# Kernel optimization log

Hardware: AMD Instinct MI355X
Metric: run time of the kernel (lower is better)

The kernel has to match this reference:

```python
import jax, jax.numpy as jnp
import numpy as np

B, L, N, D = 128, 256, 64, 1024  # batch, text_len, img_num, feat size (text=obj=place=D)


def masked_softmax(logits, mask=None):
    # matches MaskedSoftmax(dim=1): softmax over last axis, then renormalize by mask
    dist = jax.nn.softmax(logits, axis=-1)
    if mask is None:
        return dist
    dist = dist * mask
    return dist / jnp.sum(dist, axis=-1, keepdims=True)


def setup_inputs() -> dict:
    key = jax.random.key(0)
    ks = jax.random.split(key, 32)
    s = lambda d: 1.0 / np.sqrt(d)
    inp = {
        'text_feat': jax.random.normal(ks[0], (B, D), jnp.float32),
        'text_feats': jax.random.normal(ks[1], (B, L, D), jnp.float32),
        'img_object_feat': jax.random.normal(ks[2], (B, D), jnp.float32),
        'img_object_feats': jax.random.normal(ks[3], (B, N, D), jnp.float32),
        'img_place_feat': jax.random.normal(ks[4], (B, D), jnp.float32),
        'img_place_feats': jax.random.normal(ks[5], (B, N, D), jnp.float32),
        'src_mask': (jax.random.uniform(ks[6], (B, L)) < 0.9).astype(jnp.float32).at[:, 0].set(1.0),
        # score vectors (nn.Linear(D,1,bias=False))
        'v_to': jax.random.uniform(ks[7], (D,), jnp.float32, -s(D), s(D)),
        'v_tp': jax.random.uniform(ks[8], (D,), jnp.float32, -s(D), s(D)),
        'v_io': jax.random.uniform(ks[9], (D,), jnp.float32, -s(D), s(D)),
        'v_ip': jax.random.uniform(ks[10], (D,), jnp.float32, -s(D), s(D)),
        # cross-modal projections (bias=False), torch layout [out,in]
        'W_t2o': jax.random.uniform(ks[11], (D, D), jnp.float32, -s(D), s(D)),
        'W_t2p': jax.random.uniform(ks[12], (D, D), jnp.float32, -s(D), s(D)),
        'W_o2t': jax.random.uniform(ks[13], (D, D), jnp.float32, -s(D), s(D)),
        'W_p2t': jax.random.uniform(ks[14], (D, D), jnp.float32, -s(D), s(D)),
        # self projections with bias
        'W_oo': jax.random.uniform(ks[15], (D, D), jnp.float32, -s(D), s(D)),
        'b_oo': jax.random.uniform(ks[16], (D,), jnp.float32, -s(D), s(D)),
        'W_pp': jax.random.uniform(ks[17], (D, D), jnp.float32, -s(D), s(D)),
        'b_pp': jax.random.uniform(ks[18], (D,), jnp.float32, -s(D), s(D)),
        'W_tot': jax.random.uniform(ks[19], (D, D), jnp.float32, -s(D), s(D)),
        'b_tot': jax.random.uniform(ks[20], (D,), jnp.float32, -s(D), s(D)),
        'W_tpt': jax.random.uniform(ks[21], (D, D), jnp.float32, -s(D), s(D)),
        'b_tpt': jax.random.uniform(ks[22], (D,), jnp.float32, -s(D), s(D)),
        # output linear: in = 2*D + D + D = 4D
        'W_out': jax.random.uniform(ks[23], (D, 4 * D), jnp.float32, -s(4 * D), s(4 * D)),
        'b_out': jax.random.uniform(ks[24], (D,), jnp.float32, -s(4 * D), s(4 * D)),
    }
    return inp


def _text_att_ctx(text_feat, img_feats, W_img2text, W_text, b_text, v):
    # additive attention of text over image regions
    e = jnp.tanh(jnp.einsum('bnd,td->bnt', img_feats, W_img2text)
                 + (text_feat @ W_text.T + b_text)[:, None, :])
    scores = jnp.einsum('bnt,t->bn', e, v)
    dist = masked_softmax(scores)
    return jnp.einsum('bn,bnd->bd', dist, img_feats)


def _img_att_ctx(img_feat, text_feats, W_text2img, W_img, b_img, v, mask):
    e = jnp.tanh(jnp.einsum('bld,id->bli', text_feats, W_text2img)
                 + (img_feat @ W_img.T + b_img)[:, None, :])
    scores = jnp.einsum('bli,i->bl', e, v)
    dist = masked_softmax(scores, mask)
    return jnp.einsum('bl,bld->bd', dist, text_feats)


def reference(text_feat, text_feats, img_object_feat, img_object_feats, img_place_feat,
              img_place_feats, src_mask, v_to, v_tp, v_io, v_ip, W_t2o, W_t2p, W_o2t,
              W_p2t, W_oo, b_oo, W_pp, b_pp, W_tot, b_tot, W_tpt, b_tpt, W_out, b_out):
    img_object_context = _text_att_ctx(text_feat, img_object_feats, W_o2t, W_tot, b_tot, v_to)
    img_place_context = _text_att_ctx(text_feat, img_place_feats, W_p2t, W_tpt, b_tpt, v_tp)
    text_object_context = _img_att_ctx(img_object_feat, text_feats, W_t2o, W_oo, b_oo, v_io, src_mask)
    text_place_context = _img_att_ctx(img_place_feat, text_feats, W_t2p, W_pp, b_pp, v_ip, src_mask)
    combined = jnp.concatenate([img_object_context, img_place_context,
                                text_object_context, text_place_context], axis=1)
    # dropout is identity at inference
    return combined @ W_out.T + b_out
```

## Files before the change

### kernel.cpp

```cpp
#include <hip/hip_runtime.h>
#include <hip/hip_bf16.h>

typedef __attribute__((ext_vector_type(8))) short bf16x8;
typedef __attribute__((ext_vector_type(4))) float f32x4;

__device__ __forceinline__ uint pack_bf16x2(float a, float b) {
    __hip_bfloat162 p = __float22bfloat162_rn(make_float2(a, b));
    union { __hip_bfloat162 h; uint u; } c; c.h = p; return c.u;
}
__device__ __forceinline__ float bfu(ushort u) { return __uint_as_float(((uint)u) << 16); }

__device__ __forceinline__ float fast_tanh(float x) {
    float e = __expf(2.f * x);
    return 1.f - 2.f * __builtin_amdgcn_rcpf(e + 1.f);
}

__device__ __forceinline__ float wredmax(float v) {
    #pragma unroll
    for (int o = 32; o; o >>= 1) v = fmaxf(v, __shfl_xor(v, o, 64));
    return v;
}
__device__ __forceinline__ float wredsum(float v) {
    #pragma unroll
    for (int o = 32; o; o >>= 1) v += __shfl_xor(v, o, 64);
    return v;
}

__device__ __forceinline__ void gload16(const void* g, void* l) {
    __builtin_amdgcn_global_load_lds(
        (const __attribute__((address_space(1))) void*)g,
        (__attribute__((address_space(3))) void*)l, 16, 0, 0);
}

struct CvtTab {
    const float* src[8];
    ushort* dst[8];
    unsigned cum[9];
};

__global__ void cvt_bf16(CvtTab t, unsigned total4) {
    unsigned stride = gridDim.x * blockDim.x;
    for (unsigned i = blockIdx.x * blockDim.x + threadIdx.x; i < total4; i += stride) {
        int j = 0;
        while (i >= t.cum[j + 1]) ++j;
        unsigned off = i - t.cum[j];
        float4 v = reinterpret_cast<const float4*>(t.src[j])[off];
        uint2 o;
        o.x = pack_bf16x2(v.x, v.y);
        o.y = pack_bf16x2(v.z, v.w);
        reinterpret_cast<uint2*>(t.dst[j])[off] = o;
    }
}

struct Cvt8Tab {
    const float* src[8];
    uchar* dst[8];
    unsigned cum[9];
};

__device__ __forceinline__ uint pk8(float4 v) {
    int r = __builtin_amdgcn_cvt_pk_fp8_f32(v.x, v.y, 0, false);
    r = __builtin_amdgcn_cvt_pk_fp8_f32(v.z, v.w, r, true);
    return (uint)r;
}

__global__ void cvt_fp8(Cvt8Tab t, unsigned total16) {
    unsigned stride = gridDim.x * blockDim.x;
    for (unsigned i = blockIdx.x * blockDim.x + threadIdx.x; i < total16; i += stride) {
        int j = 0;
        while (i >= t.cum[j + 1]) ++j;
        unsigned off = i - t.cum[j];
        const float4* s = reinterpret_cast<const float4*>(t.src[j]) + (size_t)off * 4;
        uint4 o;
        o.x = pk8(s[0]); o.y = pk8(s[1]); o.z = pk8(s[2]); o.w = pk8(s[3]);
        *reinterpret_cast<uint4*>(t.dst[j] + (size_t)off * 16) = o;
    }
}

struct PArgs {
    const uchar* A[2];
    const uchar* Wa[2];
    const uchar* Wb[2];
    const float* qa[2];
    const float* qb[2];
    const float* va[2];
    const float* vb[2];
    float* oa[2];
    float* ob[2];
};

__global__ __launch_bounds__(512, 1) void gemm_pipe8(PArgs P, int nmul, int nbadd,
                                                     int bshift, int brshift)
{
    extern __shared__ char smem[];

    const int tid = threadIdx.x;
    const int lane = tid & 63, wv = tid >> 6;
    const int wr = wv >> 2, wc = wv & 3;
    const int lrow = lane & 15, lk = lane >> 4;

    const int br = blockIdx.x >> brshift;
    const int m0 = (blockIdx.x & ((1 << brshift) - 1)) << 8;
    const int na = blockIdx.y * nmul;
    const int nb = na + nbadd;

    const uchar* A  = P.A[br];
    const uchar* Wa = P.Wa[br];
    const uchar* Wb = P.Wb[br];

    const int rr = tid >> 2;
    const int c  = (tid & 3) ^ ((tid >> 3) & 3);
    const uchar* sA0 = A  + (size_t)(m0 + rr) * 1024 + c * 16;
    const uchar* sA1 = A  + (size_t)(m0 + 128 + rr) * 1024 + c * 16;
    const uchar* sW0 = Wa + (size_t)(na + rr) * 1024 + c * 16;
    const uchar* sW1 = Wb + (size_t)(nb + rr) * 1024 + c * 16;

    auto stage = [&](int t, int d) {
        char* b = smem + d * 32768 + tid * 16;
        size_t k = (size_t)t * 64;
        gload16(sA0 + k, b);
        gload16(sA1 + k, b + 8192);
        gload16(sW0 + k, b + 16384);
        gload16(sW1 + k, b + 24576);
    };

    auto rdA = [&](int d, int ks, int mi) -> long {
        int row = wr * 128 + mi * 16 + lrow;
        int slot = (ks << 1) | (lk >> 1);
        return *(const long*)(smem + d * 32768 + row * 64 +
                              ((slot ^ ((row >> 1) & 3)) << 4) + ((lk & 1) << 3));
    };
    auto rdB = [&](int d, int ks, int ni) -> long {
        int row = wc * 64 + ni * 16 + lrow;
        int slot = (ks << 1) | (lk >> 1);
        return *(const long*)(smem + d * 32768 + 16384 + row * 64 +
                              ((slot ^ ((row >> 1) & 3)) << 4) + ((lk & 1) << 3));
    };

    f32x4 acc[8][4];
    #pragma unroll
    for (int i = 0; i < 8; ++i)
        #pragma unroll
        for (int j = 0; j < 4; ++j) { f32x4 z = {0.f,0.f,0.f,0.f}; acc[i][j] = z; }

    stage(0, 0);
    asm volatile("s_waitcnt vmcnt(0)" ::: "memory");
    __syncthreads();

    auto body = [&](int t, int cur, int nxt, bool pf) {
        long af[4], bfr[4];
        if (pf) stage(t + 1, nxt);
        #pragma unroll
        for (int ni = 0; ni < 4; ++ni) bfr[ni] = rdB(cur, 0, ni);
        #pragma unroll
        for (int mi = 0; mi < 4; ++mi) af[mi] = rdA(cur, 0, mi);
        __builtin_amdgcn_s_setprio(1);
        #pragma unroll
        for (int mi = 0; mi < 4; ++mi)
            #pragma unroll
            for (int ni = 0; ni < 4; ++ni)
                acc[mi][ni] = __builtin_amdgcn_mfma_f32_16x16x32_fp8_fp8(af[mi], bfr[ni], acc[mi][ni], 0, 0, 0);
        __builtin_amdgcn_s_setprio(0);
        #pragma unroll
        for (int mi = 0; mi < 4; ++mi) af[mi] = rdA(cur, 0, mi + 4);
        __builtin_amdgcn_s_setprio(1);
        #pragma unroll
        for (int mi = 0; mi < 4; ++mi)
            #pragma unroll
            for (int ni = 0; ni < 4; ++ni)
                acc[mi + 4][ni] = __builtin_amdgcn_mfma_f32_16x16x32_fp8_fp8(af[mi], bfr[ni], acc[mi + 4][ni], 0, 0, 0);
        __builtin_amdgcn_s_setprio(0);
        #pragma unroll
        for (int ni = 0; ni < 4; ++ni) bfr[ni] = rdB(cur, 1, ni);
        #pragma unroll
        for (int mi = 0; mi < 4; ++mi) af[mi] = rdA(cur, 1, mi);
        __builtin_amdgcn_s_setprio(1);
        #pragma unroll
        for (int mi = 0; mi < 4; ++mi)
            #pragma unroll
            for (int ni = 0; ni < 4; ++ni)
                acc[mi][ni] = __builtin_amdgcn_mfma_f32_16x16x32_fp8_fp8(af[mi], bfr[ni], acc[mi][ni], 0, 0, 0);
        __builtin_amdgcn_s_setprio(0);
        #pragma unroll
        for (int mi = 0; mi < 4; ++mi) af[mi] = rdA(cur, 1, mi + 4);
        __builtin_amdgcn_s_setprio(1);
        #pragma unroll
        for (int mi = 0; mi < 4; ++mi)
            #pragma unroll
            for (int ni = 0; ni < 4; ++ni)
                acc[mi + 4][ni] = __builtin_amdgcn_mfma_f32_16x16x32_fp8_fp8(af[mi], bfr[ni], acc[mi + 4][ni], 0, 0, 0);
        __builtin_amdgcn_s_setprio(0);
        asm volatile("s_waitcnt vmcnt(0)" ::: "memory");
        __syncthreads();
    };

    #pragma unroll 1
    for (int tt = 0; tt < 8; ++tt) {
        body(2 * tt,     0, 1, true);
        body(2 * tt + 1, 1, 0, tt < 7);
    }

    const float* qsrc = (wc < 2) ? P.qa[br] : P.qb[br];
    const float* vsrc = (wc < 2) ? P.va[br] : P.vb[br];
    float* osrc       = (wc < 2) ? P.oa[br] : P.ob[br];
    const int nbase0 = ((wc < 2) ? na : nb) + (wc & 1) * 64;
    #pragma unroll
    for (int mi = 0; mi < 8; ++mi) {
        int mbase = m0 + wr * 128 + mi * 16;
        int bb = mbase >> bshift;
        const float* qrow = qsrc + (size_t)bb * 1024;
        float part[4] = {0.f, 0.f, 0.f, 0.f};
        #pragma unroll
        for (int ni = 0; ni < 4; ++ni) {
            int nn = nbase0 + ni * 16 + lrow;
            float qn = qrow[nn], vn = vsrc[nn];
            #pragma unroll
            for (int r2 = 0; r2 < 4; ++r2)
                part[r2] += fast_tanh(acc[mi][ni][r2] + qn) * vn;
        }
        #pragma unroll
        for (int off = 1; off < 16; off <<= 1)
            #pragma unroll
            for (int r2 = 0; r2 < 4; ++r2)
                part[r2] += __shfl_xor(part[r2], off, 64);
        if (lrow == 0) {
            #pragma unroll
            for (int r2 = 0; r2 < 4; ++r2)
                atomicAdd(&osrc[mbase + lk * 4 + r2], part[r2]);
        }
    }
}

struct QArgs {
    const ushort* A[4];
    const ushort* W[4];
    const float* bias[4];
    float* out[4];
};

__global__ __launch_bounds__(256, 2) void gemm_q(QArgs Q)
{
    __shared__ char smemq[32768];
    char* As = smemq;
    char* Ws = smemq + 16384;

    const int tid = threadIdx.x;
    const int lane = tid & 63, wv = tid >> 6, wr = wv >> 1, wc = wv & 1;
    const int lrow = lane & 15, lk = lane >> 4;
    const int n0 = blockIdx.y << 7;

    const ushort* A = Q.A[blockIdx.x];
    const ushort* W = Q.W[blockIdx.x];

    f32x4 acc[4][4];
    #pragma unroll
    for (int i = 0; i < 4; ++i)
        #pragma unroll
        for (int j = 0; j < 4; ++j) { f32x4 z = {0.f,0.f,0.f,0.f}; acc[i][j] = z; }

    const int srow = tid >> 3;
    const int g = (tid & 7) ^ (srow & 7);
    const ushort* pA = A + (size_t)srow * 1024 + g * 8;
    const ushort* pW = W + (size_t)(n0 + srow) * 1024 + g * 8;

    for (int t = 0; t < 16; ++t) {
        #pragma unroll
        for (int j = 0; j < 4; ++j)
            gload16(pA + (size_t)j * 32768 + (size_t)t * 64, As + j * 4096 + tid * 16);
        #pragma unroll
        for (int j = 0; j < 4; ++j)
            gload16(pW + (size_t)j * 32768 + (size_t)t * 64, Ws + j * 4096 + tid * 16);
        __syncthreads();
        #pragma unroll
        for (int ks = 0; ks < 2; ++ks) {
            bf16x8 af[4], bfr[4];
            const int q = ks * 4 + lk;
            #pragma unroll
            for (int mi = 0; mi < 4; ++mi) {
                int row = wr * 64 + mi * 16 + lrow;
                af[mi] = *(const bf16x8*)(As + row * 128 + ((q ^ (row & 7)) << 4));
            }
            #pragma unroll
            for (int ni = 0; ni < 4; ++ni) {
                int row = wc * 64 + ni * 16 + lrow;
                bfr[ni] = *(const bf16x8*)(Ws + row * 128 + ((q ^ (row & 7)) << 4));
            }
            #pragma unroll
            for (int mi = 0; mi < 4; ++mi)
                #pragma unroll
                for (int ni = 0; ni < 4; ++ni)
                    acc[mi][ni] = __builtin_amdgcn_mfma_f32_16x16x32_bf16(af[mi], bfr[ni], acc[mi][ni], 0, 0, 0);
        }
        __syncthreads();
    }

    float* out = Q.out[blockIdx.x];
    const float* bias = Q.bias[blockIdx.x];
    #pragma unroll
    for (int mi = 0; mi < 4; ++mi) {
        int mrow0 = wr * 64 + mi * 16 + lk * 4;
        #pragma unroll
        for (int ni = 0; ni < 4; ++ni) {
            int n = n0 + wc * 64 + ni * 16 + lrow;
            float bv = bias[n];
            #pragma unroll
            for (int r = 0; r < 4; ++r)
                out[(size_t)(mrow0 + r) * 1024 + n] = acc[mi][ni][r] + bv;
        }
    }
}

__global__ __launch_bounds__(256, 2) void gemm_fin(
    const ushort* A, const ushort* W, const float* bias, float* out, int K, int kchunk)
{
    __shared__ char smemf[32768];
    char* As = smemf;
    char* Ws = smemf + 16384;

    const int tid = threadIdx.x;
    const int lane = tid & 63, wv = tid >> 6, wr = wv >> 1, wc = wv & 1;
    const int lrow = lane & 15, lk = lane >> 4;
    const int n0 = blockIdx.y << 7;
    const int nkt = kchunk >> 6;
    const int ktbase = blockIdx.z * nkt;

    f32x4 acc[4][4];
    #pragma unroll
    for (int i = 0; i < 4; ++i)
        #pragma unroll
        for (int j = 0; j < 4; ++j) { f32x4 z = {0.f,0.f,0.f,0.f}; acc[i][j] = z; }

    const int srow = tid >> 3;
    const int g = (tid & 7) ^ (srow & 7);
    const ushort* pA = A + (size_t)srow * K + ktbase * 64 + g * 8;
    const ushort* pW = W + (size_t)(n0 + srow) * K + ktbase * 64 + g * 8;

    for (int t = 0; t < nkt; ++t) {
        #pragma unroll
        for (int j = 0; j < 4; ++j)
            gload16(pA + (size_t)j * 32 * K + (size_t)t * 64, As + j * 4096 + tid * 16);
        #pragma unroll
        for (int j = 0; j < 4; ++j)
            gload16(pW + (size_t)j * 32 * K + (size_t)t * 64, Ws + j * 4096 + tid * 16);
        __syncthreads();
        #pragma unroll
        for (int ks = 0; ks < 2; ++ks) {
            bf16x8 af[4], bfr[4];
            const int q = ks * 4 + lk;
            #pragma unroll
            for (int mi = 0; mi < 4; ++mi) {
                int row = wr * 64 + mi * 16 + lrow;
                af[mi] = *(const bf16x8*)(As + row * 128 + ((q ^ (row & 7)) << 4));
            }
            #pragma unroll
            for (int ni = 0; ni < 4; ++ni) {
                int row = wc * 64 + ni * 16 + lrow;
                bfr[ni] = *(const bf16x8*)(Ws + row * 128 + ((q ^ (row & 7)) << 4));
            }
            #pragma unroll
            for (int mi = 0; mi < 4; ++mi)
                #pragma unroll
                for (int ni = 0; ni < 4; ++ni)
                    acc[mi][ni] = __builtin_amdgcn_mfma_f32_16x16x32_bf16(af[mi], bfr[ni], acc[mi][ni], 0, 0, 0);
        }
        __syncthreads();
    }

    #pragma unroll
    for (int mi = 0; mi < 4; ++mi) {
        int mrow0 = wr * 64 + mi * 16 + lk * 4;
        #pragma unroll
        for (int ni = 0; ni < 4; ++ni) {
            int n = n0 + wc * 64 + ni * 16 + lrow;
            float bv = (blockIdx.z == 0) ? bias[n] : 0.f;
            #pragma unroll
            for (int r = 0; r < 4; ++r)
                atomicAdd(&out[(size_t)(mrow0 + r) * 1024 + n], acc[mi][ni][r] + bv);
        }
    }
}

__global__ void softmax_ctx_img(const float* __restrict__ iof, const float* __restrict__ ipf,
                                const float* __restrict__ sc_io, const float* __restrict__ sc_ip,
                                ushort* __restrict__ combined)
{
    int b = blockIdx.x, br = blockIdx.y;
    const float* A  = br ? ipf : iof;
    const float* sc = br ? sc_ip : sc_io;
    __shared__ float dist[64];
    int tid = threadIdx.x;
    if (tid < 64) {
        float s  = sc[b * 64 + tid];
        float mx = wredmax(s);
        float e  = __expf(s - mx);
        float sm = wredsum(e);
        dist[tid] = e / sm;
    }
    __syncthreads();
    int d0 = tid * 4;
    float a0 = 0, a1 = 0, a2 = 0, a3 = 0;
    const float* base = A + (size_t)b * 64 * 1024 + d0;
    #pragma unroll 4
    for (int n = 0; n < 64; ++n) {
        float w = dist[n];
        float4 t = *(const float4*)(base + (size_t)n * 1024);
        a0 += w * t.x; a1 += w * t.y; a2 += w * t.z; a3 += w * t.w;
    }
    uint2 o;
    o.x = pack_bf16x2(a0, a1);
    o.y = pack_bf16x2(a2, a3);
    *(uint2*)(combined + (size_t)b * 4096 + br * 1024 + d0) = o;
}

__global__ void softmax_ctx_text(const float* __restrict__ tf,
                                 const float* __restrict__ sc_to, const float* __restrict__ sc_tp,
                                 const float* __restrict__ mask, ushort* __restrict__ combined)
{
    int b = blockIdx.x;
    __shared__ float d3[256], d4[256], red[8];
    int tid = threadIdx.x, lane = tid & 63, wv = tid >> 6;
    float s3 = sc_to[b * 256 + tid], s4 = sc_tp[b * 256 + tid], m = mask[b * 256 + tid];
    float m3 = wredmax(s3), m4 = wredmax(s4);
    if (lane == 0) { red[wv] = m3; red[4 + wv] = m4; }
    __syncthreads();
    m3 = fmaxf(fmaxf(red[0], red[1]), fmaxf(red[2], red[3]));
    m4 = fmaxf(fmaxf(red[4], red[5]), fmaxf(red[6], red[7]));
    float e3 = __expf(s3 - m3) * m, e4 = __expf(s4 - m4) * m;
    float t3 = wredsum(e3), t4 = wredsum(e4);
    __syncthreads();
    if (lane == 0) { red[wv] = t3; red[4 + wv] = t4; }
    __syncthreads();
    t3 = red[0] + red[1] + red[2] + red[3];
    t4 = red[4] + red[5] + red[6] + red[7];
    d3[tid] = e3 / t3; d4[tid] = e4 / t4;
    __syncthreads();
    int d0 = tid * 4;
    float a0 = 0, a1 = 0, a2 = 0, a3 = 0, c0 = 0, c1 = 0, c2 = 0, c3 = 0;
    const float* base = tf + (size_t)b * 256 * 1024 + d0;
    #pragma unroll 4
    for (int l = 0; l < 256; ++l) {
        float w3 = d3[l], w4 = d4[l];
        float4 t = *(const float4*)(base + (size_t)l * 1024);
        a0 += w3 * t.x; a1 += w3 * t.y; a2 += w3 * t.z; a3 += w3 * t.w;
        c0 += w4 * t.x; c1 += w4 * t.y; c2 += w4 * t.z; c3 += w4 * t.w;
    }
    uint2 o;
    o.x = pack_bf16x2(a0, a1); o.y = pack_bf16x2(a2, a3);
    *(uint2*)(combined + (size_t)b * 4096 + 2048 + d0) = o;
    o.x = pack_bf16x2(c0, c1); o.y = pack_bf16x2(c2, c3);
    *(uint2*)(combined + (size_t)b * 4096 + 3072 + d0) = o;
}

extern "C" void kernel_launch(void* const* d_in, const int* in_sizes, int n_in,
                              void* d_out, int out_size, void* d_ws, size_t ws_size,
                              hipStream_t stream) {
    const float* text_feat        = (const float*)d_in[0];
    const float* text_feats       = (const float*)d_in[1];
    const float* img_object_feat  = (const float*)d_in[2];
    const float* img_object_feats = (const float*)d_in[3];
    const float* img_place_feat   = (const float*)d_in[4];
    const float* img_place_feats  = (const float*)d_in[5];
    const float* src_mask         = (const float*)d_in[6];
    const float* v_to  = (const float*)d_in[7];
    const float* v_tp  = (const float*)d_in[8];
    const float* v_io  = (const float*)d_in[9];
    const float* v_ip  = (const float*)d_in[10];
    const float* W_t2o = (const float*)d_in[11];
    const float* W_t2p = (const float*)d_in[12];
    const float* W_o2t = (const float*)d_in[13];
    const float* W_p2t = (const float*)d_in[14];
    const float* W_oo  = (const float*)d_in[15];
    const float* b_oo  = (const float*)d_in[16];
    const float* W_pp  = (const float*)d_in[17];
    const float* b_pp  = (const float*)d_in[18];
    const float* W_tot = (const float*)d_in[19];
    const float* b_tot = (const float*)d_in[20];
    const float* W_tpt = (const float*)d_in[21];
    const float* b_tpt = (const float*)d_in[22];
    const float* W_out = (const float*)d_in[23];
    const float* b_out = (const float*)d_in[24];

    char* p = (char*)d_ws;
    auto alloc = [&](size_t bytes) { char* r = p; p += (bytes + 255) & ~(size_t)255; return r; };
    ushort* wq_oo  = (ushort*)alloc((size_t)1024 * 1024 * 2);
    ushort* wq_pp  = (ushort*)alloc((size_t)1024 * 1024 * 2);
    ushort* wq_tot = (ushort*)alloc((size_t)1024 * 1024 * 2);
    ushort* wq_tpt = (ushort*)alloc((size_t)1024 * 1024 * 2);
    ushort* wb_out = (ushort*)alloc((size_t)1024 * 4096 * 2);
    ushort* tfq_bf  = (ushort*)alloc((size_t)128 * 1024 * 2);
    ushort* iofq_bf = (ushort*)alloc((size_t)128 * 1024 * 2);
    ushort* ipfq_bf = (ushort*)alloc((size_t)128 * 1024 * 2);
    uchar* w8_t2o = (uchar*)alloc((size_t)1024 * 1024);
    uchar* w8_t2p = (uchar*)alloc((size_t)1024 * 1024);
    uchar* w8_o2t = (uchar*)alloc((size_t)1024 * 1024);
    uchar* w8_p2t = (uchar*)alloc((size_t)1024 * 1024);
    uchar* tf8  = (uchar*)alloc((size_t)32768 * 1024);
    uchar* iof8 = (uchar*)alloc((size_t)8192 * 1024);
    uchar* ipf8 = (uchar*)alloc((size_t)8192 * 1024);
    float* q_tot = (float*)alloc((size_t)128 * 1024 * 4);
    float* q_tpt = (float*)alloc((size_t)128 * 1024 * 4);
    float* q_oo  = (float*)alloc((size_t)128 * 1024 * 4);
    float* q_pp  = (float*)alloc((size_t)128 * 1024 * 4);
    float* scores = (float*)alloc((size_t)(8192 * 2 + 32768 * 2) * 4);
    float* sc_io = scores, *sc_ip = scores + 8192, *sc_to = scores + 16384, *sc_tp = scores + 49152;
    ushort* comb_bf = (ushort*)alloc((size_t)128 * 4096 * 2);

    Cvt8Tab t8;
    const float* s8[7] = { W_t2o, W_t2p, W_o2t, W_p2t, text_feats, img_object_feats, img_place_feats };
    uchar* d8[7] = { w8_t2o, w8_t2p, w8_o2t, w8_p2t, tf8, iof8, ipf8 };
    unsigned n16[7] = { 65536, 65536, 65536, 65536, 2097152, 524288, 524288 };
    unsigned cum8 = 0;
    for (int i = 0; i < 7; ++i) { t8.src[i] = s8[i]; t8.dst[i] = d8[i]; t8.cum[i] = cum8; cum8 += n16[i]; }
    t8.src[7] = nullptr; t8.dst[7] = nullptr; t8.cum[7] = cum8; t8.cum[8] = cum8;
    cvt_fp8<<<4096, 256, 0, stream>>>(t8, cum8);

    CvtTab tb;
    const float* sb[8] = { W_oo, W_pp, W_tot, W_tpt, W_out, text_feat, img_object_feat, img_place_feat };
    ushort* db[8] = { wq_oo, wq_pp, wq_tot, wq_tpt, wb_out, tfq_bf, iofq_bf, ipfq_bf };
    unsigned nb4[8] = { 262144, 262144, 262144, 262144, 1048576, 32768, 32768, 32768 };
    unsigned cumb = 0;
    for (int i = 0; i < 8; ++i) { tb.src[i] = sb[i]; tb.dst[i] = db[i]; tb.cum[i] = cumb; cumb += nb4[i]; }
    tb.cum[8] = cumb;
    cvt_bf16<<<2048, 256, 0, stream>>>(tb, cumb);

    hipMemsetAsync(scores, 0, (size_t)(8192 * 2 + 32768 * 2) * 4, stream);
    hipMemsetAsync(d_out, 0, (size_t)128 * 1024 * 4, stream);

    QArgs qa;
    qa.A[0] = tfq_bf;  qa.W[0] = wq_tot; qa.bias[0] = b_tot; qa.out[0] = q_tot;
    qa.A[1] = tfq_bf;  qa.W[1] = wq_tpt; qa.bias[1] = b_tpt; qa.out[1] = q_tpt;
    qa.A[2] = iofq_bf; qa.W[2] = wq_oo;  qa.bias[2] = b_oo;  qa.out[2] = q_oo;
    qa.A[3] = ipfq_bf; qa.W[3] = wq_pp;  qa.bias[3] = b_pp;  qa.out[3] = q_pp;
    gemm_q<<<dim3(4, 8), 256, 0, stream>>>(qa);

    PArgs pi;
    pi.A[0] = iof8;   pi.Wa[0] = w8_o2t; pi.Wb[0] = w8_o2t;
    pi.qa[0] = q_tot; pi.qb[0] = q_tot;  pi.va[0] = v_to; pi.vb[0] = v_to;
    pi.oa[0] = sc_io; pi.ob[0] = sc_io;
    pi.A[1] = ipf8;   pi.Wa[1] = w8_p2t; pi.Wb[1] = w8_p2t;
    pi.qa[1] = q_tpt; pi.qb[1] = q_tpt;  pi.va[1] = v_tp; pi.vb[1] = v_tp;
    pi.oa[1] = sc_ip; pi.ob[1] = sc_ip;
    gemm_pipe8<<<dim3(64, 4), 512, 65536, stream>>>(pi, 256, 128, 6, 5);

    PArgs pt;
    pt.A[0] = tf8;    pt.Wa[0] = w8_t2o; pt.Wb[0] = w8_t2p;
    pt.qa[0] = q_oo;  pt.qb[0] = q_pp;   pt.va[0] = v_io; pt.vb[0] = v_ip;
    pt.oa[0] = sc_to; pt.ob[0] = sc_tp;
    pt.A[1] = pt.A[0]; pt.Wa[1] = pt.Wa[0]; pt.Wb[1] = pt.Wb[0];
    pt.qa[1] = pt.qa[0]; pt.qb[1] = pt.qb[0]; pt.va[1] = pt.va[0]; pt.vb[1] = pt.vb[0];
    pt.oa[1] = pt.oa[0]; pt.ob[1] = pt.ob[0];
    gemm_pipe8<<<dim3(128, 8), 512, 65536, stream>>>(pt, 128, 0, 8, 7);

    softmax_ctx_img<<<dim3(128, 2), 256, 0, stream>>>(img_object_feats, img_place_feats, sc_io, sc_ip, comb_bf);
    softmax_ctx_text<<<dim3(128), 256, 0, stream>>>(text_feats, sc_to, sc_tp, src_mask, comb_bf);

    gemm_fin<<<dim3(1, 8, 8), 256, 0, stream>>>(comb_bf, wb_out, b_out, (float*)d_out, 4096, 512);
}
```

Measured before the change: 308.3 us.

## Permute FP8 K layout during conversion so GEMM uses 128-bit LDS reads

The fp32-to-fp8 conversion kernel now writes each 64-wide K tile in a permuted order, so every lane's two k-steps of 8 bytes sit next to each other. The GEMM then reads both with a single 16-byte LDS load instead of two 8-byte loads and issues the two MFMAs back to back per accumulator. This halves the LDS read instruction count and removes the per-step slot computation. In exchange the conversion kernel reads less contiguous source data, and more operand registers are live at once.

```diff
diff --git a/kernel.cpp b/kernel.cpp
--- a/kernel.cpp
+++ b/kernel.cpp
@@ -3,12 +3,12 @@
 
 typedef __attribute__((ext_vector_type(8))) short bf16x8;
 typedef __attribute__((ext_vector_type(4))) float f32x4;
+typedef __attribute__((ext_vector_type(2))) long lx2;
 
 __device__ __forceinline__ uint pack_bf16x2(float a, float b) {
     __hip_bfloat162 p = __float22bfloat162_rn(make_float2(a, b));
     union { __hip_bfloat162 h; uint u; } c; c.h = p; return c.u;
 }
-__device__ __forceinline__ float bfu(ushort u) { return __uint_as_float(((uint)u) << 16); }
 
 __device__ __forceinline__ float fast_tanh(float x) {
     float e = __expf(2.f * x);
@@ -69,11 +69,16 @@
     for (unsigned i = blockIdx.x * blockDim.x + threadIdx.x; i < total16; i += stride) {
         int j = 0;
         while (i >= t.cum[j + 1]) ++j;
-        unsigned off = i - t.cum[j];
-        const float4* s = reinterpret_cast<const float4*>(t.src[j]) + (size_t)off * 4;
-        uint4 o;
-        o.x = pk8(s[0]); o.y = pk8(s[1]); o.z = pk8(s[2]); o.w = pk8(s[3]);
-        *reinterpret_cast<uint4*>(t.dst[j] + (size_t)off * 16) = o;
+        unsigned o = i - t.cum[j];
+        unsigned row = o >> 6, c = o & 63, tt = c >> 2, pp = c & 3;
+        const float* s0 = t.src[j] + (size_t)row * 1024 + tt * 64 + pp * 8;
+        float4 a0 = *(const float4*)(s0);
+        float4 a1 = *(const float4*)(s0 + 4);
+        float4 b0 = *(const float4*)(s0 + 32);
+        float4 b1 = *(const float4*)(s0 + 36);
+        uint4 ov;
+        ov.x = pk8(a0); ov.y = pk8(a1); ov.z = pk8(b0); ov.w = pk8(b1);
+        *reinterpret_cast<uint4*>(t.dst[j] + (size_t)o * 16) = ov;
     }
 }
 
@@ -124,17 +129,15 @@
         gload16(sW1 + k, b + 24576);
     };
 
-    auto rdA = [&](int d, int ks, int mi) -> long {
+    auto rdA = [&](int d, int mi) -> lx2 {
         int row = wr * 128 + mi * 16 + lrow;
-        int slot = (ks << 1) | (lk >> 1);
-        return *(const long*)(smem + d * 32768 + row * 64 +
-                              ((slot ^ ((row >> 1) & 3)) << 4) + ((lk & 1) << 3));
+        return *(const lx2*)(smem + d * 32768 + row * 64 +
+                             ((lk ^ ((row >> 1) & 3)) << 4));
     };
-    auto rdB = [&](int d, int ks, int ni) -> long {
+    auto rdB = [&](int d, int ni) -> lx2 {
         int row = wc * 64 + ni * 16 + lrow;
-        int slot = (ks << 1) | (lk >> 1);
-        return *(const long*)(smem + d * 32768 + 16384 + row * 64 +
-                              ((slot ^ ((row >> 1) & 3)) << 4) + ((lk & 1) << 3));
+        return *(const lx2*)(smem + d * 32768 + 16384 + row * 64 +
+                             ((lk ^ ((row >> 1) & 3)) << 4));
     };
 
     f32x4 acc[8][4];
@@ -148,47 +151,31 @@
     __syncthreads();
 
     auto body = [&](int t, int cur, int nxt, bool pf) {
-        long af[4], bfr[4];
+        lx2 af[4], bfr[4];
         if (pf) stage(t + 1, nxt);
         #pragma unroll
-        for (int ni = 0; ni < 4; ++ni) bfr[ni] = rdB(cur, 0, ni);
-        #pragma unroll
-        for (int mi = 0; mi < 4; ++mi) af[mi] = rdA(cur, 0, mi);
+        for (int ni = 0; ni < 4; ++ni) bfr[ni] = rdB(cur, ni);
+        #pragma unroll
+        for (int mi = 0; mi < 4; ++mi) af[mi] = rdA(cur, mi);
         __builtin_amdgcn_s_setprio(1);
         #pragma unroll
         for (int mi = 0; mi < 4; ++mi)
             #pragma unroll
-            for (int ni = 0; ni < 4; ++ni)
-                acc[mi][ni] = __builtin_amdgcn_mfma_f32_16x16x32_fp8_fp8(af[mi], bfr[ni], acc[mi][ni], 0, 0, 0);
+            for (int ni = 0; ni < 4; ++ni) {
+                acc[mi][ni] = __builtin_amdgcn_mfma_f32_16x16x32_fp8_fp8(af[mi][0], bfr[ni][0], acc[mi][ni], 0, 0, 0);
+                acc[mi][ni] = __builtin_amdgcn_mfma_f32_16x16x32_fp8_fp8(af[mi][1], bfr[ni][1], acc[mi][ni], 0, 0, 0);
+            }
         __builtin_amdgcn_s_setprio(0);
         #pragma unroll
-        for (int mi = 0; mi < 4; ++mi) af[mi] = rdA(cur, 0, mi + 4);
+        for (int mi = 0; mi < 4; ++mi) af[mi] = rdA(cur, mi + 4);
         __builtin_amdgcn_s_setprio(1);
         #pragma unroll
         for (int mi = 0; mi < 4; ++mi)
             #pragma unroll
-            for (int ni = 0; ni < 4; ++ni)
-                acc[mi + 4][ni] = __builtin_amdgcn_mfma_f32_16x16x32_fp8_fp8(af[mi], bfr[ni], acc[mi + 4][ni], 0, 0, 0);
-        __builtin_amdgcn_s_setprio(0);
-        #pragma unroll
-        for (int ni = 0; ni < 4; ++ni) bfr[ni] = rdB(cur, 1, ni);
-        #pragma unroll
-        for (int mi = 0; mi < 4; ++mi) af[mi] = rdA(cur, 1, mi);
-        __builtin_amdgcn_s_setprio(1);
-        #pragma unroll
-        for (int mi = 0; mi < 4; ++mi)
-            #pragma unroll
-            for (int ni = 0; ni < 4; ++ni)
-                acc[mi][ni] = __builtin_amdgcn_mfma_f32_16x16x32_fp8_fp8(af[mi], bfr[ni], acc[mi][ni], 0, 0, 0);
-        __builtin_amdgcn_s_setprio(0);
-        #pragma unroll
-        for (int mi = 0; mi < 4; ++mi) af[mi] = rdA(cur, 1, mi + 4);
-        __builtin_amdgcn_s_setprio(1);
-        #pragma unroll
-        for (int mi = 0; mi < 4; ++mi)
-            #pragma unroll
-            for (int ni = 0; ni < 4; ++ni)
-                acc[mi + 4][ni] = __builtin_amdgcn_mfma_f32_16x16x32_fp8_fp8(af[mi], bfr[ni], acc[mi + 4][ni], 0, 0, 0);
+            for (int ni = 0; ni < 4; ++ni) {
+                acc[mi + 4][ni] = __builtin_amdgcn_mfma_f32_16x16x32_fp8_fp8(af[mi][0], bfr[ni][0], acc[mi + 4][ni], 0, 0, 0);
+                acc[mi + 4][ni] = __builtin_amdgcn_mfma_f32_16x16x32_fp8_fp8(af[mi][1], bfr[ni][1], acc[mi + 4][ni], 0, 0, 0);
+            }
         __builtin_amdgcn_s_setprio(0);
         asm volatile("s_waitcnt vmcnt(0)" ::: "memory");
         __syncthreads();
```

New measurement: 295.6 us. -4.1%, faster.
